# Optimization experiments

Hardware: AMD Instinct MI355X
Metric: run time of the kernel (lower is better)

Reference implementation:

```python
import jax, jax.numpy as jnp
import numpy as np

N_NODES = 100000
N_EDGES = 3200000
F_IN = 128
H = 32
C = 8


def _graph_conv(x, src, dst, ew, W_rel, b_rel, W_root):
    # PyG GraphConv: sum-aggregate edge_weight * x[src] into dst, then
    # lin_rel(agg) + lin_root(x). lin_root has no bias.
    msg = x[src] * ew[:, None]                                  # [E, F]
    agg = jax.ops.segment_sum(msg, dst, num_segments=N_NODES)   # [N, F]
    return agg @ W_rel.T + b_rel + x @ W_root.T


def setup_inputs() -> dict:
    key = jax.random.key(0)
    ks = jax.random.split(key, 12)
    x = jax.random.normal(ks[0], (N_NODES, F_IN), dtype=jnp.float32)
    edge_index = jax.random.randint(ks[1], (2, N_EDGES), 0, N_NODES, dtype=jnp.int32)
    edge_weights = jax.random.uniform(ks[2], (N_EDGES,), dtype=jnp.float32)
    s = lambda fan_in: 1.0 / np.sqrt(fan_in)
    W1_rel = jax.random.uniform(ks[3], (H, F_IN), minval=-s(F_IN), maxval=s(F_IN), dtype=jnp.float32)
    b1 = jax.random.uniform(ks[4], (H,), minval=-s(F_IN), maxval=s(F_IN), dtype=jnp.float32)
    W1_root = jax.random.uniform(ks[5], (H, F_IN), minval=-s(F_IN), maxval=s(F_IN), dtype=jnp.float32)
    W2_rel = jax.random.uniform(ks[6], (H, H), minval=-s(H), maxval=s(H), dtype=jnp.float32)
    b2 = jax.random.uniform(ks[7], (H,), minval=-s(H), maxval=s(H), dtype=jnp.float32)
    W2_root = jax.random.uniform(ks[8], (H, H), minval=-s(H), maxval=s(H), dtype=jnp.float32)
    W3_rel = jax.random.uniform(ks[9], (C, H), minval=-s(H), maxval=s(H), dtype=jnp.float32)
    b3 = jax.random.uniform(ks[10], (C,), minval=-s(H), maxval=s(H), dtype=jnp.float32)
    W3_root = jax.random.uniform(ks[11], (C, H), minval=-s(H), maxval=s(H), dtype=jnp.float32)
    return {"x": x, "edge_index": edge_index, "edge_weights": edge_weights,
            "W1_rel": W1_rel, "b1": b1, "W1_root": W1_root,
            "W2_rel": W2_rel, "b2": b2, "W2_root": W2_root,
            "W3_rel": W3_rel, "b3": b3, "W3_root": W3_root}


def reference(x, edge_index, edge_weights,
              W1_rel, b1, W1_root, W2_rel, b2, W2_root, W3_rel, b3, W3_root):
    src, dst = edge_index[0], edge_index[1]
    h = _graph_conv(x, src, dst, edge_weights, W1_rel, b1, W1_root)
    h = jax.nn.leaky_relu(h, negative_slope=0.01)
    # dropout is identity in eval mode
    h = _graph_conv(h, src, dst, edge_weights, W2_rel, b2, W2_root)
    h = jax.nn.leaky_relu(h, negative_slope=0.01)
    out = _graph_conv(h, src, dst, edge_weights, W3_rel, b3, W3_root)
    return out
```

## Files before the change

kernel.cpp:

```cpp
#include <hip/hip_runtime.h>

#define NN 100000
#define NE 3200000
#define NE4 (NE / 4)
#define FIN 128
#define HD 32
#define CD 8
#define NPB 256
#define NBUCK ((NN + NPB - 1) / NPB)
#define CHUNK_B 8192

typedef unsigned int uint;
typedef unsigned short ushort;

__device__ __forceinline__ float lrelu(float v) { return v > 0.f ? v : 0.01f * v; }
__device__ __forceinline__ uint bf16rne(float x) {
    uint u = __float_as_uint(x);
    return (u + 0x7FFFu + ((u >> 16) & 1u)) >> 16;
}
__device__ __forceinline__ uint pack2(float a, float b) {
    return bf16rne(a) | (bf16rne(b) << 16);
}
__device__ __forceinline__ float lo16(uint v) { return __uint_as_float(v << 16); }
__device__ __forceinline__ float hi16(uint v) { return __uint_as_float(v & 0xFFFF0000u); }


__global__ __launch_bounds__(256) void k_proj128(
    const float* __restrict__ x, const float* __restrict__ Wrel,
    const float* __restrict__ Wroot, const float* __restrict__ b,
    uint* __restrict__ pB, float* __restrict__ R)
{
    __shared__ float Wt[FIN][64];
    for (int idx = threadIdx.x; idx < FIN * 64; idx += 256) {
        int k = idx >> 6, j = idx & 63;
        Wt[k][j] = (j < HD) ? Wrel[j * FIN + k] : Wroot[(j - HD) * FIN + k];
    }
    __syncthreads();
    int n = blockIdx.x * 256 + threadIdx.x;
    if (n >= NN) return;

    float accP[HD], accR[HD];
#pragma unroll
    for (int j = 0; j < HD; ++j) { accP[j] = 0.f; accR[j] = 0.f; }

    const float4* x4 = (const float4*)(x + (size_t)n * FIN);
#pragma unroll 2
    for (int k4 = 0; k4 < FIN / 4; ++k4) {
        float4 xv = x4[k4];
        float xs[4] = {xv.x, xv.y, xv.z, xv.w};
#pragma unroll
        for (int kk = 0; kk < 4; ++kk) {
            float xk = xs[kk];
            int k = k4 * 4 + kk;
#pragma unroll
            for (int j = 0; j < HD; ++j) {
                accP[j] += xk * Wt[k][j];
                accR[j] += xk * Wt[k][j + HD];
            }
        }
    }
    uint4* pp = (uint4*)(pB + (size_t)n * 16);
#pragma unroll
    for (int q = 0; q < 4; ++q)
        pp[q] = make_uint4(pack2(accP[8*q+0], accP[8*q+1]), pack2(accP[8*q+2], accP[8*q+3]),
                           pack2(accP[8*q+4], accP[8*q+5]), pack2(accP[8*q+6], accP[8*q+7]));
    float4* rr = (float4*)(R + (size_t)n * HD);
#pragma unroll
    for (int q = 0; q < HD / 4; ++q)
        rr[q] = make_float4(accR[4*q+0] + b[4*q+0], accR[4*q+1] + b[4*q+1],
                            accR[4*q+2] + b[4*q+2], accR[4*q+3] + b[4*q+3]);
}


__global__ __launch_bounds__(256) void k_mid(
    const float* __restrict__ G, const float* R_in,
    const float* __restrict__ Wrel, const float* __restrict__ Wroot,
    const float* __restrict__ b,
    uint* __restrict__ pB, float* R_out)
{
    __shared__ float Ws[HD][64];
    for (int idx = threadIdx.x; idx < HD * 64; idx += 256) {
        int k = idx >> 6, j = idx & 63;
        Ws[k][j] = (j < HD) ? Wrel[j * HD + k] : Wroot[(j - HD) * HD + k];
    }
    __syncthreads();
    int n = blockIdx.x * 256 + threadIdx.x;
    if (n >= NN) return;

    float h[HD];
    const float4* av = (const float4*)(G + (size_t)n * HD);
    const float4* rv = (const float4*)(R_in + (size_t)n * HD);
#pragma unroll
    for (int q = 0; q < HD / 4; ++q) {
        float4 a = av[q], r_ = rv[q];
        h[4*q+0] = lrelu(a.x + r_.x);
        h[4*q+1] = lrelu(a.y + r_.y);
        h[4*q+2] = lrelu(a.z + r_.z);
        h[4*q+3] = lrelu(a.w + r_.w);
    }
    float accP[HD], accR[HD];
#pragma unroll
    for (int j = 0; j < HD; ++j) { accP[j] = 0.f; accR[j] = 0.f; }
#pragma unroll 4
    for (int k = 0; k < HD; ++k) {
        float hk = h[k];
#pragma unroll
        for (int j = 0; j < HD; ++j) {
            accP[j] += hk * Ws[k][j];
            accR[j] += hk * Ws[k][j + HD];
        }
    }
    uint4* pp = (uint4*)(pB + (size_t)n * 16);
#pragma unroll
    for (int q = 0; q < 4; ++q)
        pp[q] = make_uint4(pack2(accP[8*q+0], accP[8*q+1]), pack2(accP[8*q+2], accP[8*q+3]),
                           pack2(accP[8*q+4], accP[8*q+5]), pack2(accP[8*q+6], accP[8*q+7]));
    float4* rr = (float4*)(R_out + (size_t)n * HD);
#pragma unroll
    for (int q = 0; q < HD / 4; ++q)
        rr[q] = make_float4(accR[4*q+0] + b[4*q+0], accR[4*q+1] + b[4*q+1],
                            accR[4*q+2] + b[4*q+2], accR[4*q+3] + b[4*q+3]);
}

__global__ __launch_bounds__(256) void k_last(
    const float* __restrict__ G, const float* __restrict__ R,
    const float* __restrict__ Wrel, const float* __restrict__ Wroot,
    const float* __restrict__ b,
    uint* __restrict__ p3B, float* __restrict__ out)
{
    __shared__ float Ws[HD][16];
    for (int idx = threadIdx.x; idx < HD * 16; idx += 256) {
        int k = idx >> 4, j = idx & 15;
        Ws[k][j] = (j < CD) ? Wrel[j * HD + k] : Wroot[(j - CD) * HD + k];
    }
    __syncthreads();
    int n = blockIdx.x * 256 + threadIdx.x;
    if (n >= NN) return;

    float h[HD];
    const float4* av = (const float4*)(G + (size_t)n * HD);
    const float4* rv = (const float4*)(R + (size_t)n * HD);
#pragma unroll
    for (int q = 0; q < HD / 4; ++q) {
        float4 a = av[q], r_ = rv[q];
        h[4*q+0] = lrelu(a.x + r_.x);
        h[4*q+1] = lrelu(a.y + r_.y);
        h[4*q+2] = lrelu(a.z + r_.z);
        h[4*q+3] = lrelu(a.w + r_.w);
    }
    float accP[CD], accR[CD];
#pragma unroll
    for (int j = 0; j < CD; ++j) { accP[j] = 0.f; accR[j] = 0.f; }
#pragma unroll
    for (int k = 0; k < HD; ++k) {
        float hk = h[k];
#pragma unroll
        for (int j = 0; j < CD; ++j) {
            accP[j] += hk * Ws[k][j];
            accR[j] += hk * Ws[k][j + CD];
        }
    }
    uint4* pp = (uint4*)(p3B + (size_t)n * 4);
    pp[0] = make_uint4(pack2(accP[0], accP[1]), pack2(accP[2], accP[3]),
                       pack2(accP[4], accP[5]), pack2(accP[6], accP[7]));
    float4* oo = (float4*)(out + (size_t)n * CD);
    oo[0] = make_float4(accR[0] + b[0], accR[1] + b[1], accR[2] + b[2], accR[3] + b[3]);
    oo[1] = make_float4(accR[4] + b[4], accR[5] + b[5], accR[6] + b[6], accR[7] + b[7]);
}


__global__ __launch_bounds__(512) void k_bhist(
    const int* __restrict__ dst, int* __restrict__ bcnt)
{
    __shared__ int lc[NBUCK];
    int t = threadIdx.x;
    for (int i = t; i < NBUCK; i += 512) lc[i] = 0;
    __syncthreads();
    const int4* dst4 = (const int4*)dst;
    for (int i4 = blockIdx.x * 512 + t; i4 < NE4; i4 += gridDim.x * 512) {
        int4 d = dst4[i4];
        atomicAdd(&lc[d.x >> 8], 1);
        atomicAdd(&lc[d.y >> 8], 1);
        atomicAdd(&lc[d.z >> 8], 1);
        atomicAdd(&lc[d.w >> 8], 1);
    }
    __syncthreads();
    for (int i = t; i < NBUCK; i += 512) {
        int c = lc[i];
        if (c) atomicAdd(&bcnt[i], c);
    }
}

__global__ __launch_bounds__(512) void k_bscan(
    const int* __restrict__ bcnt, int* __restrict__ bbase, int* __restrict__ bcur)
{
    __shared__ int s[512];
    int t = threadIdx.x;
    s[t] = (t < NBUCK) ? bcnt[t] : 0;
    __syncthreads();
    for (int off = 1; off < 512; off <<= 1) {
        int a = (t >= off) ? s[t - off] : 0;
        __syncthreads();
        s[t] += a;
        __syncthreads();
    }
    int excl = t ? s[t - 1] : 0;
    if (t < NBUCK) { bbase[t] = excl; bcur[t] = excl; }
    if (t == 0) bbase[NBUCK] = NE;
}

__global__ __launch_bounds__(512) void k_bscatter(
    const int* __restrict__ src, const int* __restrict__ dst, const float* __restrict__ ew,
    int* __restrict__ bcur, int2* __restrict__ tmp)
{
    __shared__ int hist[NBUCK];
    __shared__ int s[512];
    __shared__ int off[NBUCK];
    __shared__ int cur[NBUCK];
    __shared__ ushort perm[CHUNK_B];
    int t = threadIdx.x;
    int base = blockIdx.x * CHUNK_B;
    int cnt = min(CHUNK_B, NE - base);

    for (int i = t; i < NBUCK; i += 512) hist[i] = 0;
    __syncthreads();
    for (int i = t; i < cnt; i += 512)
        atomicAdd(&hist[dst[base + i] >> 8], 1);
    __syncthreads();
    s[t] = (t < NBUCK) ? hist[t] : 0;
    __syncthreads();
    for (int o = 1; o < 512; o <<= 1) {
        int a = (t >= o) ? s[t - o] : 0;
        __syncthreads();
        s[t] += a;
        __syncthreads();
    }
    if (t < NBUCK) {
        int excl = t ? s[t - 1] : 0;
        int c = hist[t];
        int g = c ? atomicAdd(&bcur[t], c) : 0;
        off[t] = g - excl;
        cur[t] = excl;
    }
    __syncthreads();
    for (int i = t; i < cnt; i += 512) {
        int b = dst[base + i] >> 8;
        int r = atomicAdd(&cur[b], 1);
        perm[r] = (ushort)i;
    }
    __syncthreads();
    for (int i = t; i < cnt; i += 512) {
        int e = base + (int)perm[i];
        int d = dst[e];
        tmp[off[d >> 8] + i] = make_int2(src[e] | ((d & 255) << 17), __float_as_int(ew[e]));
    }
}

__global__ __launch_bounds__(512) void k_bsort(
    const int* __restrict__ bbase, const int2* __restrict__ tmp,
    int2* __restrict__ epack, int* __restrict__ rowstart)
{
    int b = blockIdx.x, t = threadIdx.x;
    int lo = bbase[b], hi = bbase[b + 1], cnt = hi - lo;
    __shared__ int hist[NPB];
    __shared__ int sc[NPB];
    __shared__ int cur[NPB];
    if (t < NPB) hist[t] = 0;
    __syncthreads();
    for (int i = t; i < cnt; i += 512)
        atomicAdd(&hist[(tmp[lo + i].x >> 17) & 255], 1);
    __syncthreads();
    if (t < NPB) sc[t] = hist[t];
    __syncthreads();
    for (int off = 1; off < NPB; off <<= 1) {
        int a = (t < NPB && t >= off) ? sc[t - off] : 0;
        __syncthreads();
        if (t < NPB) sc[t] += a;
        __syncthreads();
    }
    if (t < NPB) {
        int excl = t ? sc[t - 1] : 0;
        int node = (b << 8) + t;
        if (node < NN) rowstart[node] = lo + excl;
        cur[t] = lo + excl;
    }
    if (b == 0 && t == 0) rowstart[NN] = NE;
    __syncthreads();
    for (int i = t; i < cnt; i += 512) {
        int2 v = tmp[lo + i];
        int l = (v.x >> 17) & 255;
        int pos = atomicAdd(&cur[l], 1);
        epack[pos] = make_int2(v.x & 0x1FFFF, v.y);
    }
}


__global__ __launch_bounds__(256) void k_gather32(
    const int* __restrict__ rowstart, const int2* __restrict__ epack,
    const uint* __restrict__ pB, float* __restrict__ G)
{
    int wid = (blockIdx.x * 256 + threadIdx.x) >> 6;
    if (wid >= NN) return;
    int lane = threadIdx.x & 63;
    int q = lane >> 4, f2 = lane & 15;
    int rs = rowstart[wid], re = rowstart[wid + 1];

    float a0 = 0.f, a1 = 0.f, b0 = 0.f, b1 = 0.f;
    int e = rs + q;
    for (; e + 4 < re; e += 8) {
        int2 p0 = epack[e];
        int2 p1 = epack[e + 4];
        uint v0 = pB[((size_t)p0.x << 4) + f2];
        uint v1 = pB[((size_t)p1.x << 4) + f2];
        float w0 = __int_as_float(p0.y), w1 = __int_as_float(p1.y);
        a0 += lo16(v0) * w0; a1 += hi16(v0) * w0;
        b0 += lo16(v1) * w1; b1 += hi16(v1) * w1;
    }
    for (; e < re; e += 4) {
        int2 p0 = epack[e];
        uint v0 = pB[((size_t)p0.x << 4) + f2];
        float w0 = __int_as_float(p0.y);
        a0 += lo16(v0) * w0; a1 += hi16(v0) * w0;
    }
    a0 += b0; a1 += b1;
    a0 += __shfl_xor(a0, 16); a1 += __shfl_xor(a1, 16);
    a0 += __shfl_xor(a0, 32); a1 += __shfl_xor(a1, 32);
    if (lane < 16) {
        float2* g2 = (float2*)(G + (size_t)wid * HD + 2 * f2);
        *g2 = make_float2(a0, a1);
    }
}

__global__ __launch_bounds__(256) void k_gather8(
    const int* __restrict__ rowstart, const int2* __restrict__ epack,
    const uint* __restrict__ p3B, float* __restrict__ out)
{
    int wid = (blockIdx.x * 256 + threadIdx.x) >> 6;
    if (wid >= NN) return;
    int lane = threadIdx.x & 63;
    int q = lane >> 2, f2 = lane & 3;
    int rs = rowstart[wid], re = rowstart[wid + 1];

    float a0 = 0.f, a1 = 0.f, b0 = 0.f, b1 = 0.f;
    int e = rs + q;
    for (; e + 16 < re; e += 32) {
        int2 p0 = epack[e];
        int2 p1 = epack[e + 16];
        uint v0 = p3B[((size_t)p0.x << 2) + f2];
        uint v1 = p3B[((size_t)p1.x << 2) + f2];
        float w0 = __int_as_float(p0.y), w1 = __int_as_float(p1.y);
        a0 += lo16(v0) * w0; a1 += hi16(v0) * w0;
        b0 += lo16(v1) * w1; b1 += hi16(v1) * w1;
    }
    for (; e < re; e += 16) {
        int2 p0 = epack[e];
        uint v0 = p3B[((size_t)p0.x << 2) + f2];
        float w0 = __int_as_float(p0.y);
        a0 += lo16(v0) * w0; a1 += hi16(v0) * w0;
    }
    a0 += b0; a1 += b1;
    a0 += __shfl_xor(a0, 4);  a1 += __shfl_xor(a1, 4);
    a0 += __shfl_xor(a0, 8);  a1 += __shfl_xor(a1, 8);
    a0 += __shfl_xor(a0, 16); a1 += __shfl_xor(a1, 16);
    a0 += __shfl_xor(a0, 32); a1 += __shfl_xor(a1, 32);
    if (lane < 4) {
        float2* o2 = (float2*)(out + (size_t)wid * CD + 2 * f2);
        float2 t = *o2;
        t.x += a0; t.y += a1;
        *o2 = t;
    }
}


extern "C" void kernel_launch(void* const* d_in, const int* in_sizes, int n_in,
                              void* d_out, int out_size, void* d_ws, size_t ws_size,
                              hipStream_t stream)
{
    const float* x      = (const float*)d_in[0];
    const int*   ei     = (const int*)d_in[1];
    const float* ew     = (const float*)d_in[2];
    const float* W1rel  = (const float*)d_in[3];
    const float* b1     = (const float*)d_in[4];
    const float* W1root = (const float*)d_in[5];
    const float* W2rel  = (const float*)d_in[6];
    const float* b2     = (const float*)d_in[7];
    const float* W2root = (const float*)d_in[8];
    const float* W3rel  = (const float*)d_in[9];
    const float* b3     = (const float*)d_in[10];
    const float* W3root = (const float*)d_in[11];
    float* out = (float*)d_out;

    const int* src = ei;
    const int* dst = ei + NE;

    char* ws = (char*)d_ws;
    int2*  epack    = (int2*)ws;   ws += (size_t)NE * sizeof(int2);
    char*  unionA   = ws;          ws += (size_t)NE * sizeof(int2);
    uint*  pB       = (uint*)ws;   ws += (size_t)NN * 16 * 4;
    uint*  p3B      = (uint*)ws;   ws += (size_t)NN * 4 * 4;
    int*   rowstart = (int*)ws;    ws += (size_t)(NN + 1) * 4;
    int*   bcnt     = (int*)ws;    ws += (size_t)NBUCK * 4;
    int*   bbase    = (int*)ws;    ws += (size_t)(NBUCK + 1) * 4;
    int*   bcur     = (int*)ws;

    int2*  tmp = (int2*)unionA;
    float* G   = (float*)unionA;
    float* R   = G + (size_t)NN * HD;

    const int nodeBlocks = (NN + 255) / 256;
    const int waveBlocks = (NN + 3) / 4;
    const int scatBlocks = (NE + CHUNK_B - 1) / CHUNK_B;

    hipMemsetAsync(bcnt, 0, (size_t)NBUCK * 4, stream);
    k_bhist<<<512, 512, 0, stream>>>(dst, bcnt);
    k_bscan<<<1, 512, 0, stream>>>(bcnt, bbase, bcur);
    k_bscatter<<<scatBlocks, 512, 0, stream>>>(src, dst, ew, bcur, tmp);
    k_bsort<<<NBUCK, 512, 0, stream>>>(bbase, tmp, epack, rowstart);

    k_proj128<<<nodeBlocks, 256, 0, stream>>>(x, W1rel, W1root, b1, pB, R);
    k_gather32<<<waveBlocks, 256, 0, stream>>>(rowstart, epack, pB, G);
    k_mid<<<nodeBlocks, 256, 0, stream>>>(G, R, W2rel, W2root, b2, pB, R);
    k_gather32<<<waveBlocks, 256, 0, stream>>>(rowstart, epack, pB, G);
    k_last<<<nodeBlocks, 256, 0, stream>>>(G, R, W3rel, W3root, b3, p3B, out);
    k_gather8<<<waveBlocks, 256, 0, stream>>>(rowstart, epack, p3B, out);
}
```

Before: 462.0 us.

## Halve CSR bucket size, shrink scatter chunk, unroll gather32 to four edges

Node buckets for the counting sort shrink from 256 to 128 nodes, which doubles the bucket count to about 782. The scans now handle two buckets per thread, and the scatter chunk drops to 4096 edges. This gives the sort kernel smaller and more numerous blocks, at the cost of more global atomics and more scatter blocks. Separately, the 32-wide gather loop is unrolled to four independent edge loads per thread to raise memory-level parallelism, using more registers.

```diff
diff --git a/kernel.cpp b/kernel.cpp
--- a/kernel.cpp
+++ b/kernel.cpp
@@ -6,9 +6,9 @@
 #define FIN 128
 #define HD 32
 #define CD 8
-#define NPB 256
+#define NPB 128
 #define NBUCK ((NN + NPB - 1) / NPB)
-#define CHUNK_B 8192
+#define CHUNK_B 4096
 
 typedef unsigned int uint;
 typedef unsigned short ushort;
@@ -179,10 +179,10 @@
     const int4* dst4 = (const int4*)dst;
     for (int i4 = blockIdx.x * 512 + t; i4 < NE4; i4 += gridDim.x * 512) {
         int4 d = dst4[i4];
-        atomicAdd(&lc[d.x >> 8], 1);
-        atomicAdd(&lc[d.y >> 8], 1);
-        atomicAdd(&lc[d.z >> 8], 1);
-        atomicAdd(&lc[d.w >> 8], 1);
+        atomicAdd(&lc[d.x >> 7], 1);
+        atomicAdd(&lc[d.y >> 7], 1);
+        atomicAdd(&lc[d.z >> 7], 1);
+        atomicAdd(&lc[d.w >> 7], 1);
     }
     __syncthreads();
     for (int i = t; i < NBUCK; i += 512) {
@@ -196,7 +196,10 @@
 {
     __shared__ int s[512];
     int t = threadIdx.x;
-    s[t] = (t < NBUCK) ? bcnt[t] : 0;
+    int i0 = 2 * t, i1 = 2 * t + 1;
+    int a0 = (i0 < NBUCK) ? bcnt[i0] : 0;
+    int a1 = (i1 < NBUCK) ? bcnt[i1] : 0;
+    s[t] = a0 + a1;
     __syncthreads();
     for (int off = 1; off < 512; off <<= 1) {
         int a = (t >= off) ? s[t - off] : 0;
@@ -204,8 +207,9 @@
         s[t] += a;
         __syncthreads();
     }
-    int excl = t ? s[t - 1] : 0;
-    if (t < NBUCK) { bbase[t] = excl; bcur[t] = excl; }
+    int ex = t ? s[t - 1] : 0;
+    if (i0 < NBUCK) { bbase[i0] = ex; bcur[i0] = ex; }
+    if (i1 < NBUCK) { bbase[i1] = ex + a0; bcur[i1] = ex + a0; }
     if (t == 0) bbase[NBUCK] = NE;
 }
 
@@ -214,7 +218,7 @@
     int* __restrict__ bcur, int2* __restrict__ tmp)
 {
     __shared__ int hist[NBUCK];
-    __shared__ int s[512];
+    __shared__ int s2[512];
     __shared__ int off[NBUCK];
     __shared__ int cur[NBUCK];
     __shared__ ushort perm[CHUNK_B];
@@ -225,26 +229,34 @@
     for (int i = t; i < NBUCK; i += 512) hist[i] = 0;
     __syncthreads();
     for (int i = t; i < cnt; i += 512)
-        atomicAdd(&hist[dst[base + i] >> 8], 1);
-    __syncthreads();
-    s[t] = (t < NBUCK) ? hist[t] : 0;
+        atomicAdd(&hist[dst[base + i] >> 7], 1);
+    __syncthreads();
+    int i0 = 2 * t, i1 = 2 * t + 1;
+    int c0 = (i0 < NBUCK) ? hist[i0] : 0;
+    int c1 = (i1 < NBUCK) ? hist[i1] : 0;
+    s2[t] = c0 + c1;
     __syncthreads();
     for (int o = 1; o < 512; o <<= 1) {
-        int a = (t >= o) ? s[t - o] : 0;
-        __syncthreads();
-        s[t] += a;
-        __syncthreads();
-    }
-    if (t < NBUCK) {
-        int excl = t ? s[t - 1] : 0;
-        int c = hist[t];
-        int g = c ? atomicAdd(&bcur[t], c) : 0;
-        off[t] = g - excl;
-        cur[t] = excl;
+        int a = (t >= o) ? s2[t - o] : 0;
+        __syncthreads();
+        s2[t] += a;
+        __syncthreads();
+    }
+    int ex = t ? s2[t - 1] : 0;
+    if (i0 < NBUCK) {
+        int g = c0 ? atomicAdd(&bcur[i0], c0) : 0;
+        off[i0] = g - ex;
+        cur[i0] = ex;
+    }
+    if (i1 < NBUCK) {
+        int ex1 = ex + c0;
+        int g = c1 ? atomicAdd(&bcur[i1], c1) : 0;
+        off[i1] = g - ex1;
+        cur[i1] = ex1;
     }
     __syncthreads();
     for (int i = t; i < cnt; i += 512) {
-        int b = dst[base + i] >> 8;
+        int b = dst[base + i] >> 7;
         int r = atomicAdd(&cur[b], 1);
         perm[r] = (ushort)i;
     }
@@ -252,7 +264,7 @@
     for (int i = t; i < cnt; i += 512) {
         int e = base + (int)perm[i];
         int d = dst[e];
-        tmp[off[d >> 8] + i] = make_int2(src[e] | ((d & 255) << 17), __float_as_int(ew[e]));
+        tmp[off[d >> 7] + i] = make_int2(src[e] | ((d & 127) << 17), __float_as_int(ew[e]));
     }
 }
 
@@ -268,7 +280,7 @@
     if (t < NPB) hist[t] = 0;
     __syncthreads();
     for (int i = t; i < cnt; i += 512)
-        atomicAdd(&hist[(tmp[lo + i].x >> 17) & 255], 1);
+        atomicAdd(&hist[(tmp[lo + i].x >> 17) & 127], 1);
     __syncthreads();
     if (t < NPB) sc[t] = hist[t];
     __syncthreads();
@@ -280,7 +292,7 @@
     }
     if (t < NPB) {
         int excl = t ? sc[t - 1] : 0;
-        int node = (b << 8) + t;
+        int node = (b << 7) + t;
         if (node < NN) rowstart[node] = lo + excl;
         cur[t] = lo + excl;
     }
@@ -288,7 +300,7 @@
     __syncthreads();
     for (int i = t; i < cnt; i += 512) {
         int2 v = tmp[lo + i];
-        int l = (v.x >> 17) & 255;
+        int l = (v.x >> 17) & 127;
         int pos = atomicAdd(&cur[l], 1);
         epack[pos] = make_int2(v.x & 0x1FFFF, v.y);
     }
@@ -306,15 +318,23 @@
     int rs = rowstart[wid], re = rowstart[wid + 1];
 
     float a0 = 0.f, a1 = 0.f, b0 = 0.f, b1 = 0.f;
+    float c0 = 0.f, c1 = 0.f, d0 = 0.f, d1 = 0.f;
     int e = rs + q;
-    for (; e + 4 < re; e += 8) {
+    for (; e + 12 < re; e += 16) {
         int2 p0 = epack[e];
         int2 p1 = epack[e + 4];
+        int2 p2 = epack[e + 8];
+        int2 p3 = epack[e + 12];
         uint v0 = pB[((size_t)p0.x << 4) + f2];
         uint v1 = pB[((size_t)p1.x << 4) + f2];
+        uint v2 = pB[((size_t)p2.x << 4) + f2];
+        uint v3 = pB[((size_t)p3.x << 4) + f2];
         float w0 = __int_as_float(p0.y), w1 = __int_as_float(p1.y);
+        float w2 = __int_as_float(p2.y), w3 = __int_as_float(p3.y);
         a0 += lo16(v0) * w0; a1 += hi16(v0) * w0;
         b0 += lo16(v1) * w1; b1 += hi16(v1) * w1;
+        c0 += lo16(v2) * w2; c1 += hi16(v2) * w2;
+        d0 += lo16(v3) * w3; d1 += hi16(v3) * w3;
     }
     for (; e < re; e += 4) {
         int2 p0 = epack[e];
@@ -322,7 +342,7 @@
         float w0 = __int_as_float(p0.y);
         a0 += lo16(v0) * w0; a1 += hi16(v0) * w0;
     }
-    a0 += b0; a1 += b1;
+    a0 += b0 + c0 + d0; a1 += b1 + c1 + d1;
     a0 += __shfl_xor(a0, 16); a1 += __shfl_xor(a1, 16);
     a0 += __shfl_xor(a0, 32); a1 += __shfl_xor(a1, 32);
     if (lane < 16) {
```

Result: slower. 477.8 us (+3.4%).
